# Performance work log

Hardware: AMD Instinct MI355X
Metric: run time of the kernel (lower is better)

## Reference

```python
import jax, jax.numpy as jnp
from jax import lax
import numpy as np

N_SEGMENT = 8
N_DIV = 4
C = 256
NT = 64  # n_batch(8) * n_segment(8)
H = W = 56


def _ms_weights(planes, n_div):
    fold = planes // n_div
    w1 = np.zeros((planes, 1, 1, 1, 1), np.float32); w1[:, 0, 0] = 1.0
    w3 = np.zeros((planes, 1, 3, 1, 1), np.float32)
    w3[:fold, 0, 0] = 1.0; w3[fold:2 * fold, 0, 2] = 1.0; w3[2 * fold:, 0, 1] = 1.0
    w5 = np.zeros((planes, 1, 5, 1, 1), np.float32)
    w5[:fold, 0, :2] = 1.0; w5[fold:2 * fold, 0, 3:] = 1.0; w5[2 * fold:, 0, 2] = 1.0
    w7 = np.zeros((planes, 1, 7, 1, 1), np.float32)
    w7[:fold, 0, :3] = 1.0; w7[fold:2 * fold, 0, 4:] = 1.0; w7[2 * fold:, 0, 3] = 1.0
    return w1, w3, w5, w7


def setup_inputs() -> dict:
    key = jax.random.key(0)
    kx, kn = jax.random.split(key)
    x = jax.random.normal(kx, (NT, C, H, W), dtype=jnp.float32)
    w1, w3, w5, w7 = _ms_weights(C // 4, N_DIV)
    net_w = jax.random.normal(kn, (C, C, 1, 1), dtype=jnp.float32) * (1.0 / np.sqrt(C))
    return {
        "x": x,
        "w1": jnp.asarray(w1), "w3": jnp.asarray(w3),
        "w5": jnp.asarray(w5), "w7": jnp.asarray(w7),
        "net_w": net_w,
    }


def _dw_temporal_conv3d(x, w, pad):
    # x: (n, c4, T, h, w); w: (c4, 1, K, 1, 1) depthwise over temporal dim
    return lax.conv_general_dilated(
        x, w, window_strides=(1, 1, 1),
        padding=[(pad, pad), (0, 0), (0, 0)],
        dimension_numbers=("NCDHW", "OIDHW", "NCDHW"),
        feature_group_count=x.shape[1])


def reference(x, w1, w3, w5, w7, net_w):
    nt, c, h, wd = x.shape
    n = nt // N_SEGMENT
    c4 = c // 4
    # (nt,c,h,w) -> (n, c, T, h, w)
    xv = x.reshape(n, N_SEGMENT, c, h, wd).transpose(0, 2, 1, 3, 4)
    ws = (w1, w3, w5, w7)
    pads = (0, 1, 2, 3)
    ys = [_dw_temporal_conv3d(xv[:, i * c4:(i + 1) * c4], ws[i], pads[i])
          for i in range(4)]
    y = jnp.concatenate(ys, axis=1)                       # (n, c, T, h, w)
    y = y.transpose(0, 2, 1, 3, 4).reshape(nt, c, h, wd)  # back to (nt,c,h,w)
    # wrapped net: bias-free 1x1 Conv2d
    out = lax.conv_general_dilated(
        y, net_w, window_strides=(1, 1), padding="VALID",
        dimension_numbers=("NCHW", "OIHW", "NCHW"))
    return out
```

## Files before the change

kernel.cpp:

```cpp
#include <hip/hip_runtime.h>

#define HW 3136
#define C_ 256
#define T_ 8
#define NPOS 64
#define NBLK_PER_NT 49
#define YSTRIDE 40

typedef __attribute__((ext_vector_type(8))) short bf16x8;
typedef __attribute__((ext_vector_type(4))) float f32x4;
typedef __attribute__((ext_vector_type(4))) unsigned int u32x4;
typedef __attribute__((ext_vector_type(4))) int i32x4;

__device__ __forceinline__ unsigned short f2bf(float f) {
  unsigned int u = __float_as_uint(f);
  u += 0x7FFF + ((u >> 16) & 1);
  return (unsigned short)(u >> 16);
}

struct TapC { float w0, w1, w2; int dts; };


__global__ void prep_kernel(const float* __restrict__ w1, const float* __restrict__ w3,
                            const float* __restrict__ w5, const float* __restrict__ w7,
                            const float* __restrict__ net_w,
                            unsigned short* __restrict__ Wb, TapC* __restrict__ tab) {
  int tid = blockIdx.x * blockDim.x + threadIdx.x;
  for (int i = tid; i < C_ * C_; i += gridDim.x * blockDim.x)
    Wb[i] = f2bf(net_w[i]);
  if (tid < C_) {
    int c = tid, g = c >> 6, lc = c & 63, K = 2 * g + 1;
    const float* wsrc = (g == 0) ? w1 : (g == 1) ? w3 : (g == 2) ? w5 : w7;
    float w[3] = {0.f, 0.f, 0.f};
    int d[3] = {0, 0, 0};
    int cnt = 0;
    for (int k = 0; k < K && cnt < 3; ++k) {
      float v = wsrc[lc * K + k];
      if (v != 0.0f) { d[cnt] = k - g; w[cnt] = v; cnt++; }
    }
    TapC tc;
    tc.w0 = w[0]; tc.w1 = w[1]; tc.w2 = w[2];
    tc.dts = (d[0] + 4) | ((d[1] + 4) << 8) | ((d[2] + 4) << 16);
    tab[c] = tc;
  }
}

__global__ __launch_bounds__(256, 4) void fused_kernel(
    const float* __restrict__ x, const unsigned short* __restrict__ Wb,
    const TapC* __restrict__ tab, float* __restrict__ out) {
  const int blk = blockIdx.x;
  const int nt = blk / NBLK_PER_NT;
  const int p0 = (blk % NBLK_PER_NT) * NPOS;
  const int n = nt >> 3, t = nt & 7;
  const int tid = threadIdx.x;
  const int lane = tid & 63;
  const int wv = tid >> 6;
  const int m16 = lane & 15;
  const int quad = lane >> 4;

  __shared__ __align__(16) unsigned short ylds[2][NPOS * YSTRIDE];
  __shared__ __align__(16) TapC ltab[C_];

  ltab[tid & (C_ - 1)] = tab[tid & (C_ - 1)];

  f32x4 acc[4][4];
#pragma unroll
  for (int i = 0; i < 4; ++i)
#pragma unroll
    for (int j = 0; j < 4; ++j) acc[i][j] = (f32x4){0.f, 0.f, 0.f, 0.f};

  const int pp = tid & 63;
  const int chunk = tid >> 6;

  const float* xbase = x + (size_t)(n * 8) * C_ * HW + (size_t)(p0 + pp);

  __syncthreads();

  for (int ks = 0; ks < 8; ++ks) {
    const int cbase = ks * 32 + chunk * 8;
    float xv[8][3];
    float wk[8][3];
#pragma unroll
    for (int j = 0; j < 8; ++j) {
      const int c = cbase + j;
      const TapC tc = ltab[c];
      const float tw[3] = {tc.w0, tc.w1, tc.w2};
#pragma unroll
      for (int s = 0; s < 3; ++s) {
        const int dt = ((tc.dts >> (8 * s)) & 0xFF) - 4;
        const int tq = t + dt;
        const bool ok = (unsigned)tq < (unsigned)T_;
        const int tqc = ok ? tq : t;
        wk[j][s] = ok ? tw[s] : 0.f;
        xv[j][s] = xbase[(size_t)((tqc * C_ + c) * HW)];
      }
    }
    unsigned short pk[8];
#pragma unroll
    for (int j = 0; j < 8; ++j) {
      float a = wk[j][0] * xv[j][0] + wk[j][1] * xv[j][1] + wk[j][2] * xv[j][2];
      pk[j] = f2bf(a);
    }
    const int buf = ks & 1;
    *(u32x4*)&ylds[buf][pp * YSTRIDE + chunk * 8] = *(const u32x4*)pk;
    __syncthreads();
    const int k0 = ks * 32;
#pragma unroll
    for (int ni = 0; ni < 4; ++ni) {
      const bf16x8 bfrag = *(const bf16x8*)&ylds[buf][(ni * 16 + m16) * YSTRIDE + quad * 8];
#pragma unroll
      for (int mi = 0; mi < 4; ++mi) {
        const int oc = wv * 64 + mi * 16 + m16;
        const bf16x8 afrag = *(const bf16x8*)&Wb[oc * C_ + k0 + quad * 8];
        acc[mi][ni] =
            __builtin_amdgcn_mfma_f32_16x16x32_bf16(afrag, bfrag, acc[mi][ni], 0, 0, 0);
      }
    }
  }

  const size_t obase = (size_t)nt * C_ * HW + p0 + m16;
#pragma unroll
  for (int mi = 0; mi < 4; ++mi) {
#pragma unroll
    for (int r = 0; r < 4; ++r) {
      const int oc = wv * 64 + mi * 16 + quad * 4 + r;
      float* orow = out + obase + (size_t)oc * HW;
#pragma unroll
      for (int ni = 0; ni < 4; ++ni) orow[ni * 16] = acc[mi][ni][r];
    }
  }
}

extern "C" void kernel_launch(void* const* d_in, const int* in_sizes, int n_in,
                              void* d_out, int out_size, void* d_ws, size_t ws_size,
                              hipStream_t stream) {
  const float* x = (const float*)d_in[0];
  const float* w1 = (const float*)d_in[1];
  const float* w3 = (const float*)d_in[2];
  const float* w5 = (const float*)d_in[3];
  const float* w7 = (const float*)d_in[4];
  const float* net_w = (const float*)d_in[5];
  float* out = (float*)d_out;

  char* ws = (char*)d_ws;
  unsigned short* Wb = (unsigned short*)ws;
  TapC* tab = (TapC*)(ws + 131072);

  hipLaunchKernelGGL(prep_kernel, dim3(64), dim3(256), 0, stream,
                     w1, w3, w5, w7, net_w, Wb, tab);
  hipLaunchKernelGGL(fused_kernel, dim3(64 * NBLK_PER_NT), dim3(256), 0, stream,
                     x, Wb, tab, out);
}
```

Before: 434.8 us.

## Fold temporal shift weights into GEMM K dimension and prefetch x loads

Replaces the per-channel three-tap temporal reduction with an expanded K dimension of 352 slots. Each nonzero tap becomes its own GEMM column, and the tap weight is folded into a precomputed bf16 1x1 weight matrix. Per-timestep row offset tables with an invalid flag replace the on-the-fly tap math, and x loads for the next K step are software-pipelined into a double register buffer. This trades fewer redundant global loads and less ALU work for a larger K (11 steps instead of 8), an extra prep launch, and bf16 rounding of the product weights.

After: 407.5 us. 1.07x faster.

```diff
diff --git a/kernel.cpp b/kernel.cpp
--- a/kernel.cpp
+++ b/kernel.cpp
@@ -6,6 +6,9 @@
 #define NPOS 64
 #define NBLK_PER_NT 49
 #define YSTRIDE 40
+#define KP 352
+#define NKS 11
+#define FLAGBIT 0x40000000
 
 typedef __attribute__((ext_vector_type(8))) short bf16x8;
 typedef __attribute__((ext_vector_type(4))) float f32x4;
@@ -18,36 +21,60 @@
   return (unsigned short)(u >> 16);
 }
 
-struct TapC { float w0, w1, w2; int dts; };
 
-
-__global__ void prep_kernel(const float* __restrict__ w1, const float* __restrict__ w3,
-                            const float* __restrict__ w5, const float* __restrict__ w7,
-                            const float* __restrict__ net_w,
-                            unsigned short* __restrict__ Wb, TapC* __restrict__ tab) {
-  int tid = blockIdx.x * blockDim.x + threadIdx.x;
-  for (int i = tid; i < C_ * C_; i += gridDim.x * blockDim.x)
-    Wb[i] = f2bf(net_w[i]);
-  if (tid < C_) {
-    int c = tid, g = c >> 6, lc = c & 63, K = 2 * g + 1;
-    const float* wsrc = (g == 0) ? w1 : (g == 1) ? w3 : (g == 2) ? w5 : w7;
-    float w[3] = {0.f, 0.f, 0.f};
-    int d[3] = {0, 0, 0};
-    int cnt = 0;
-    for (int k = 0; k < K && cnt < 3; ++k) {
-      float v = wsrc[lc * K + k];
-      if (v != 0.0f) { d[cnt] = k - g; w[cnt] = v; cnt++; }
+__global__ void prep_table(const float* __restrict__ w1, const float* __restrict__ w3,
+                           const float* __restrict__ w5, const float* __restrict__ w7,
+                           int* __restrict__ slotC, float* __restrict__ slotW,
+                           int* __restrict__ rowtab) {
+  const int c = threadIdx.x;
+  for (int s = c; s < KP; s += 256) {
+    slotC[s] = 0;
+    slotW[s] = 0.f;
+    for (int t = 0; t < T_; ++t) rowtab[t * KP + s] = 0;
+  }
+  const int g = c >> 6, lc = c & 63, K = 2 * g + 1;
+  const float* wsrc = (g == 0) ? w1 : (g == 1) ? w3 : (g == 2) ? w5 : w7;
+  float w[3] = {0.f, 0.f, 0.f};
+  int d[3] = {0, 0, 0};
+  int cnt = 0;
+  for (int k = 0; k < K && cnt < 3; ++k) {
+    float v = wsrc[lc * K + k];
+    if (v != 0.0f) { w[cnt] = v; d[cnt] = k - g; ++cnt; }
+  }
+  __shared__ int ps[256];
+  ps[c] = cnt;
+  __syncthreads();
+  for (int dlt = 1; dlt < 256; dlt <<= 1) {
+    int v = (c >= dlt) ? ps[c - dlt] : 0;
+    __syncthreads();
+    ps[c] += v;
+    __syncthreads();
+  }
+  const int off = ps[c] - cnt;
+  for (int i = 0; i < cnt; ++i) {
+    const int s = off + i;
+    if (s >= KP) break;
+    slotC[s] = c;
+    slotW[s] = w[i];
+    for (int t = 0; t < T_; ++t) {
+      const int tq = t + d[i];
+      const bool valid = (unsigned)tq < (unsigned)T_;
+      const int tqc = valid ? tq : (tq < 0 ? 0 : T_ - 1);
+      rowtab[t * KP + s] = ((tqc * C_ + c) * HW) | (valid ? 0 : FLAGBIT);
     }
-    TapC tc;
-    tc.w0 = w[0]; tc.w1 = w[1]; tc.w2 = w[2];
-    tc.dts = (d[0] + 4) | ((d[1] + 4) << 8) | ((d[2] + 4) << 16);
-    tab[c] = tc;
   }
 }
 
+__global__ void prep_wb(const float* __restrict__ net_w, const int* __restrict__ slotC,
+                        const float* __restrict__ slotW, unsigned short* __restrict__ Wbp) {
+  const int oc = blockIdx.x;
+  const int s = threadIdx.x;
+  if (s < KP) Wbp[oc * KP + s] = f2bf(net_w[oc * C_ + slotC[s]] * slotW[s]);
+}
+
 __global__ __launch_bounds__(256, 4) void fused_kernel(
-    const float* __restrict__ x, const unsigned short* __restrict__ Wb,
-    const TapC* __restrict__ tab, float* __restrict__ out) {
+    const float* __restrict__ x, const unsigned short* __restrict__ Wbp,
+    const int* __restrict__ rowtab, float* __restrict__ out) {
   const int blk = blockIdx.x;
   const int nt = blk / NBLK_PER_NT;
   const int p0 = (blk % NBLK_PER_NT) * NPOS;
@@ -57,11 +84,13 @@
   const int wv = tid >> 6;
   const int m16 = lane & 15;
   const int quad = lane >> 4;
+  const int pp = tid & 63;
+  const int chunk = tid >> 6;
 
   __shared__ __align__(16) unsigned short ylds[2][NPOS * YSTRIDE];
-  __shared__ __align__(16) TapC ltab[C_];
+  __shared__ __align__(16) int ltab[KP];
 
-  ltab[tid & (C_ - 1)] = tab[tid & (C_ - 1)];
+  for (int i = tid; i < KP; i += 256) ltab[i] = rowtab[t * KP + i];
 
   f32x4 acc[4][4];
 #pragma unroll
@@ -69,52 +98,57 @@
 #pragma unroll
     for (int j = 0; j < 4; ++j) acc[i][j] = (f32x4){0.f, 0.f, 0.f, 0.f};
 
-  const int pp = tid & 63;
-  const int chunk = tid >> 6;
-
-  const float* xbase = x + (size_t)(n * 8) * C_ * HW + (size_t)(p0 + pp);
+  const float* xn = x + (size_t)(n * 8) * C_ * HW + (size_t)(p0 + pp);
 
   __syncthreads();
 
-  for (int ks = 0; ks < 8; ++ks) {
-    const int cbase = ks * 32 + chunk * 8;
-    float xv[8][3];
-    float wk[8][3];
+  float xv[2][8];
+  {
+    const i32x4 o0 = *(const i32x4*)&ltab[chunk * 8];
+    const i32x4 o1 = *(const i32x4*)&ltab[chunk * 8 + 4];
 #pragma unroll
-    for (int j = 0; j < 8; ++j) {
-      const int c = cbase + j;
-      const TapC tc = ltab[c];
-      const float tw[3] = {tc.w0, tc.w1, tc.w2};
+    for (int j = 0; j < 4; ++j) {
+      const int ofa = o0[j];
+      const float va = xn[ofa & (FLAGBIT - 1)];
+      xv[0][j] = (ofa & FLAGBIT) ? 0.f : va;
+      const int ofb = o1[j];
+      const float vb = xn[ofb & (FLAGBIT - 1)];
+      xv[0][4 + j] = (ofb & FLAGBIT) ? 0.f : vb;
+    }
+  }
+
 #pragma unroll
-      for (int s = 0; s < 3; ++s) {
-        const int dt = ((tc.dts >> (8 * s)) & 0xFF) - 4;
-        const int tq = t + dt;
-        const bool ok = (unsigned)tq < (unsigned)T_;
-        const int tqc = ok ? tq : t;
-        wk[j][s] = ok ? tw[s] : 0.f;
-        xv[j][s] = xbase[(size_t)((tqc * C_ + c) * HW)];
+  for (int ks = 0; ks < NKS; ++ks) {
+    const int buf = ks & 1;
+    bf16x8 af[4];
+#pragma unroll
+    for (int mi = 0; mi < 4; ++mi)
+      af[mi] = *(const bf16x8*)&Wbp[(size_t)((wv * 64 + mi * 16 + m16) * KP) + ks * 32 + quad * 8];
+    unsigned short pk[8];
+#pragma unroll
+    for (int j = 0; j < 8; ++j) pk[j] = f2bf(xv[buf][j]);
+    *(u32x4*)&ylds[buf][pp * YSTRIDE + chunk * 8] = *(const u32x4*)pk;
+    if (ks + 1 < NKS) {
+      const i32x4 o0 = *(const i32x4*)&ltab[(ks + 1) * 32 + chunk * 8];
+      const i32x4 o1 = *(const i32x4*)&ltab[(ks + 1) * 32 + chunk * 8 + 4];
+#pragma unroll
+      for (int j = 0; j < 4; ++j) {
+        const int ofa = o0[j];
+        const float va = xn[ofa & (FLAGBIT - 1)];
+        xv[buf ^ 1][j] = (ofa & FLAGBIT) ? 0.f : va;
+        const int ofb = o1[j];
+        const float vb = xn[ofb & (FLAGBIT - 1)];
+        xv[buf ^ 1][4 + j] = (ofb & FLAGBIT) ? 0.f : vb;
       }
     }
-    unsigned short pk[8];
-#pragma unroll
-    for (int j = 0; j < 8; ++j) {
-      float a = wk[j][0] * xv[j][0] + wk[j][1] * xv[j][1] + wk[j][2] * xv[j][2];
-      pk[j] = f2bf(a);
-    }
-    const int buf = ks & 1;
-    *(u32x4*)&ylds[buf][pp * YSTRIDE + chunk * 8] = *(const u32x4*)pk;
     __syncthreads();
-    const int k0 = ks * 32;
 #pragma unroll
     for (int ni = 0; ni < 4; ++ni) {
       const bf16x8 bfrag = *(const bf16x8*)&ylds[buf][(ni * 16 + m16) * YSTRIDE + quad * 8];
 #pragma unroll
-      for (int mi = 0; mi < 4; ++mi) {
-        const int oc = wv * 64 + mi * 16 + m16;
-        const bf16x8 afrag = *(const bf16x8*)&Wb[oc * C_ + k0 + quad * 8];
+      for (int mi = 0; mi < 4; ++mi)
         acc[mi][ni] =
-            __builtin_amdgcn_mfma_f32_16x16x32_bf16(afrag, bfrag, acc[mi][ni], 0, 0, 0);
-      }
+            __builtin_amdgcn_mfma_f32_16x16x32_bf16(af[mi], bfrag, acc[mi][ni], 0, 0, 0);
     }
   }
 
@@ -143,11 +177,14 @@
   float* out = (float*)d_out;
 
   char* ws = (char*)d_ws;
-  unsigned short* Wb = (unsigned short*)ws;
-  TapC* tab = (TapC*)(ws + 131072);
+  unsigned short* Wbp = (unsigned short*)ws;
+  int* slotC = (int*)(ws + 180224);
+  float* slotW = (float*)(ws + 181632);
+  int* rowtab = (int*)(ws + 183040);
 
-  hipLaunchKernelGGL(prep_kernel, dim3(64), dim3(256), 0, stream,
-                     w1, w3, w5, w7, net_w, Wb, tab);
+  hipLaunchKernelGGL(prep_table, dim3(1), dim3(256), 0, stream, w1, w3, w5, w7,
+                     slotC, slotW, rowtab);
+  hipLaunchKernelGGL(prep_wb, dim3(C_), dim3(384), 0, stream, net_w, slotC, slotW, Wbp);
   hipLaunchKernelGGL(fused_kernel, dim3(64 * NBLK_PER_NT), dim3(256), 0, stream,
-                     x, Wb, tab, out);
+                     x, Wbp, rowtab, out);
 }
```
